# Kernel tuning notes

Hardware: AMD Instinct MI355X
Metric: run time of the kernel (lower is better)

The kernel has to match this reference:

```python
import jax, jax.numpy as jnp
import numpy as np

B, T, D_IN, H, E = 256, 512, 256, 256, 96  # batch, enc seq, input_size, hidden_size, num_embeddings


def setup_inputs() -> dict:
    key = jax.random.key(0)
    ks = jax.random.split(key, 12)
    s = 0.05
    return {
        "prev_h": jax.random.normal(ks[0], (B, H), jnp.float32),
        "prev_c": jax.random.normal(ks[1], (B, H), jnp.float32),
        "batch_H": jax.random.normal(ks[2], (B, T, D_IN), jnp.float32),
        "char_onehots": jax.random.uniform(ks[3], (B, E), jnp.float32),
        "W_i2h": jax.random.normal(ks[4], (H, D_IN), jnp.float32) * s,
        "W_h2h": jax.random.normal(ks[5], (H, H), jnp.float32) * s,
        "b_h2h": jax.random.normal(ks[6], (H,), jnp.float32) * s,
        "W_score": jax.random.normal(ks[7], (1, H), jnp.float32) * s,
        "W_ih": jax.random.normal(ks[8], (4 * H, D_IN + E), jnp.float32) * s,
        "W_hh": jax.random.normal(ks[9], (4 * H, H), jnp.float32) * s,
        "b_ih": jax.random.normal(ks[10], (4 * H,), jnp.float32) * s,
        "b_hh": jax.random.normal(ks[11], (4 * H,), jnp.float32) * s,
    }


def reference(prev_h, prev_c, batch_H, char_onehots,
              W_i2h, W_h2h, b_h2h, W_score, W_ih, W_hh, b_ih, b_hh):
    # additive attention over encoder features
    proj = jnp.einsum('btd,hd->bth', batch_H, W_i2h)          # [B,T,H]
    hid = prev_h @ W_h2h.T + b_h2h                             # [B,H]
    e = jnp.einsum('bth,oh->bto', jnp.tanh(proj + hid[:, None, :]), W_score)  # [B,T,1]
    alpha = jax.nn.softmax(e, axis=1)                          # [B,T,1]
    context = jnp.einsum('bt,btd->bd', alpha[..., 0], batch_H) # [B,D_IN]
    x = jnp.concatenate([context, char_onehots], axis=1)       # [B,D_IN+E]
    # LSTM cell step (PyTorch gate order: i, f, g, o)
    gates = x @ W_ih.T + b_ih + prev_h @ W_hh.T + b_hh         # [B,4H]
    i, f, g, o = jnp.split(gates, 4, axis=1)
    c_new = jax.nn.sigmoid(f) * prev_c + jax.nn.sigmoid(i) * jnp.tanh(g)
    h_new = jax.nn.sigmoid(o) * jnp.tanh(c_new)
    return (h_new, c_new, jnp.swapaxes(alpha, 1, 2))           # alpha -> [B,1,T]
```

## Files before the change

kernel.cpp:

```cpp
#include <hip/hip_runtime.h>

typedef __attribute__((ext_vector_type(8))) short short8;
typedef __attribute__((ext_vector_type(4))) float f32x4;

#define KPAD 40
#define APITCH 264

#define WS_HID   0u
#define WS_P     262144u
#define WS_Z     786432u
#define WS_CTX   794624u
#define WS_CTXP  1056768u
#define WS_WBF   3153920u

__device__ __forceinline__ unsigned cvtpk(float lo, float hi) {
    unsigned r;
    asm("v_cvt_pk_bf16_f32 %0, %1, %2" : "=v"(r) : "v"(lo), "v"(hi));
    return r;
}
__device__ __forceinline__ int4 pack8(float4 x0, float4 x1) {
    int4 q;
    q.x = (int)cvtpk(x0.x, x0.y);
    q.y = (int)cvtpk(x0.z, x0.w);
    q.z = (int)cvtpk(x1.x, x1.y);
    q.w = (int)cvtpk(x1.z, x1.w);
    return q;
}
__device__ __forceinline__ float bf2f(unsigned s) {
    union { float f; unsigned u; } v; v.u = s << 16;
    return v.f;
}
__device__ __forceinline__ float tanh_fast(float x) {
    float e2 = __expf(2.f * x);
    return 1.f - 2.f * __builtin_amdgcn_rcpf(e2 + 1.f);
}
__device__ __forceinline__ float sigmoid_fast(float x) {
    return __builtin_amdgcn_rcpf(1.f + __expf(-x));
}

__global__ __launch_bounds__(256) void k_prep(
    const float* __restrict__ prev_h, const float* __restrict__ W_i2h,
    const float* __restrict__ W_h2h, const float* __restrict__ b_h2h,
    float* __restrict__ hid, short* __restrict__ Wbf)
{
    int bid = blockIdx.x, tid = threadIdx.x;
    if (bid < 256) {
        __shared__ float ph[256];
        ph[tid] = prev_h[bid * 256 + tid];
        __syncthreads();
        float acc = b_h2h[tid];
        const float4* w = (const float4*)(W_h2h + tid * 256);
        #pragma unroll 8
        for (int k4 = 0; k4 < 64; ++k4) {
            float4 ww = w[k4];
            acc += ww.x * ph[k4*4+0] + ww.y * ph[k4*4+1] + ww.z * ph[k4*4+2] + ww.w * ph[k4*4+3];
        }
        hid[bid * 256 + tid] = acc;
    } else {
        int idx = ((bid - 256) * 256 + tid) * 8;
        float4 x0 = *(const float4*)(W_i2h + idx);
        float4 x1 = *(const float4*)(W_i2h + idx + 4);
        *(int4*)&Wbf[idx] = pack8(x0, x1);
    }
}

__global__ __launch_bounds__(256, 2) void k_escore_ctx(
    const float* __restrict__ BH, const short* __restrict__ Wbf,
    const float* __restrict__ hid, const float* __restrict__ Wsc,
    float* __restrict__ p_out, float* __restrict__ zbuf, float* __restrict__ ctxp)
{
    __shared__ short Al[64 * APITCH];
    __shared__ float eps[4 * 64];
    __shared__ float pl[64];
    __shared__ float r4[4 * 256];

    const int tid = threadIdx.x;
    const int lane = tid & 63;
    const int w = tid >> 6;
    const int l15 = lane & 15, lg = lane >> 4;
    const int bt0 = blockIdx.x * 64;
    const int b = bt0 >> 9;
    const int c = blockIdx.x & 7;

    short8 breg[4][8];
    {
        const short* bb = Wbf + (size_t)(w * 64 + l15) * 256 + lg * 8;
        #pragma unroll
        for (int cf = 0; cf < 4; cf++)
            #pragma unroll
            for (int ks = 0; ks < 8; ks++)
                breg[cf][ks] = *(const short8*)(bb + (size_t)cf * 16 * 256 + ks * 32);
    }

    {
        const float* as = BH + (size_t)bt0 * 256 + tid * 8;
        const int row0 = tid >> 5, colw = (tid & 31) * 8;
        #pragma unroll
        for (int i = 0; i < 8; ++i) {
            float4 x0 = *(const float4*)(as + i * 2048);
            float4 x1 = *(const float4*)(as + i * 2048 + 4);
            *(int4*)&Al[(i * 8 + row0) * APITCH + colw] = pack8(x0, x1);
        }
    }
    __syncthreads();

    f32x4 acc[4][4];
    #pragma unroll
    for (int i = 0; i < 4; i++)
        #pragma unroll
        for (int j = 0; j < 4; j++) acc[i][j] = (f32x4){0.f, 0.f, 0.f, 0.f};

    #pragma unroll
    for (int ks = 0; ks < 8; ++ks) {
        short8 af[4];
        #pragma unroll
        for (int rf = 0; rf < 4; rf++)
            af[rf] = *(const short8*)&Al[(rf * 16 + l15) * APITCH + ks * 32 + lg * 8];
        #pragma unroll
        for (int rf = 0; rf < 4; rf++)
            #pragma unroll
            for (int cf = 0; cf < 4; cf++)
                acc[rf][cf] = __builtin_amdgcn_mfma_f32_16x16x32_bf16(af[rf], breg[cf][ks], acc[rf][cf], 0, 0, 0);
    }

    float esum[4][4];
    #pragma unroll
    for (int rf = 0; rf < 4; rf++)
        #pragma unroll
        for (int r = 0; r < 4; r++) esum[rf][r] = 0.f;

    #pragma unroll
    for (int cf = 0; cf < 4; cf++) {
        int col = w * 64 + cf * 16 + l15;
        float wsv = Wsc[col];
        float hd = hid[b * 256 + col];
        #pragma unroll
        for (int rf = 0; rf < 4; rf++)
            #pragma unroll
            for (int r = 0; r < 4; r++)
                esum[rf][r] += wsv * tanh_fast(acc[rf][cf][r] + hd);
    }
    #pragma unroll
    for (int rf = 0; rf < 4; rf++)
        #pragma unroll
        for (int r = 0; r < 4; r++) {
            float s = esum[rf][r];
            s += __shfl_xor(s, 1); s += __shfl_xor(s, 2);
            s += __shfl_xor(s, 4); s += __shfl_xor(s, 8);
            esum[rf][r] = s;
        }
    if (l15 == 0) {
        #pragma unroll
        for (int rf = 0; rf < 4; rf++)
            #pragma unroll
            for (int r = 0; r < 4; r++)
                eps[w * 64 + rf * 16 + lg * 4 + r] = esum[rf][r];
    }
    __syncthreads();

    if (tid < 64) {
        float e = eps[tid] + eps[64 + tid] + eps[128 + tid] + eps[192 + tid];
        float p = __expf(e);
        p_out[bt0 + tid] = p;
        pl[tid] = p;
        float z = p;
        z += __shfl_xor(z, 1); z += __shfl_xor(z, 2); z += __shfl_xor(z, 4);
        z += __shfl_xor(z, 8); z += __shfl_xor(z, 16); z += __shfl_xor(z, 32);
        if (tid == 0) zbuf[blockIdx.x] = z;
    }
    __syncthreads();

    {
        float c0 = 0.f, c1 = 0.f, c2 = 0.f, c3 = 0.f;
        #pragma unroll
        for (int t = 0; t < 16; ++t) {
            int row = w * 16 + t;
            float pv = pl[row];
            unsigned v1 = *(const unsigned*)&Al[row * APITCH + lane * 2];
            unsigned v2 = *(const unsigned*)&Al[row * APITCH + 128 + lane * 2];
            c0 += pv * bf2f(v1 & 0xffffu); c1 += pv * bf2f(v1 >> 16);
            c2 += pv * bf2f(v2 & 0xffffu); c3 += pv * bf2f(v2 >> 16);
        }
        r4[w * 256 + lane * 2]       = c0;
        r4[w * 256 + lane * 2 + 1]   = c1;
        r4[w * 256 + 128 + lane * 2] = c2;
        r4[w * 256 + 129 + lane * 2] = c3;
    }
    __syncthreads();
    ctxp[((size_t)(c * 256 + b)) * 256 + tid] = r4[tid] + r4[256 + tid] + r4[512 + tid] + r4[768 + tid];
}

__global__ __launch_bounds__(256) void k_finalize(
    const float* __restrict__ p, const float* __restrict__ zbuf,
    const float* __restrict__ ctxp, float* __restrict__ alpha, float* __restrict__ ctx)
{
    int b = blockIdx.x, t = threadIdx.x;
    float Z = 0.f;
    #pragma unroll
    for (int cc = 0; cc < 8; ++cc) Z += zbuf[b * 8 + cc];
    float inv = 1.f / Z;
    alpha[b * 512 + t] = p[b * 512 + t] * inv;
    alpha[b * 512 + 256 + t] = p[b * 512 + 256 + t] * inv;
    float s = 0.f;
    #pragma unroll
    for (int cc = 0; cc < 8; ++cc) s += ctxp[((size_t)(cc * 256 + b)) * 256 + t];
    ctx[b * 256 + t] = s * inv;
}

__global__ __launch_bounds__(256) void k_gates_lstm(
    const float* __restrict__ ctx, const float* __restrict__ onehot,
    const float* __restrict__ prev_h, const float* __restrict__ W_ih,
    const float* __restrict__ W_hh, const float* __restrict__ b_ih,
    const float* __restrict__ b_hh, const float* __restrict__ prev_c,
    float* __restrict__ out)
{
    __shared__ char smem[20800];
    short* AlB = (short*)smem;
    short* BlB = (short*)smem + 5120;
    const int tid = threadIdx.x;
    const int lane = tid & 63;
    const int w = tid >> 6;
    const int l15 = lane & 15, lg = lane >> 4;
    const int rb = blockIdx.x * 64;
    const int hb = blockIdx.y;

    f32x4 acc[4];
    #pragma unroll
    for (int j = 0; j < 4; j++) acc[j] = (f32x4){0.f, 0.f, 0.f, 0.f};

    const int arow = tid >> 2, akg = tid & 3;
    const int rg = rb + arow;
    const int bn = tid >> 2, bq = tid & 3;
    const int np_ = hb * 64 + bn, hh_ = np_ >> 2, gg_ = np_ & 3;
    const float* wih_row = W_ih + (size_t)(gg_ * 256 + hh_) * 352;
    const float* whh_row = W_hh + (size_t)(gg_ * 256 + hh_) * 256;

    auto stageAB = [&](int kc, int bu) {
        int k0 = kc * 32 + akg * 8;
        const float4* pa;
        if (k0 < 256)      pa = (const float4*)(ctx    + rg * 256 + k0);
        else if (k0 < 352) pa = (const float4*)(onehot + rg * 96  + (k0 - 256));
        else               pa = (const float4*)(prev_h + rg * 256 + (k0 - 352));
        float4 x0 = pa[0], x1 = pa[1];
        *(int4*)&AlB[bu * 2560 + arow * KPAD + akg * 8] = pack8(x0, x1);
        int kb = kc * 32 + bq * 8;
        const float* pb = (kb < 352) ? (wih_row + kb) : (whh_row + (kb - 352));
        float4 y0 = *(const float4*)pb, y1 = *(const float4*)(pb + 4);
        *(int4*)&BlB[bu * 2560 + bn * KPAD + bq * 8] = pack8(y0, y1);
    };

    stageAB(0, 0);
    __syncthreads();

    for (int kc = 0; kc < 19; ++kc) {
        int cur = kc & 1;
        short8 af = *(const short8*)&AlB[cur * 2560 + (w * 16 + l15) * KPAD + lg * 8];
        short8 bfr[4];
        #pragma unroll
        for (int cf = 0; cf < 4; cf++)
            bfr[cf] = *(const short8*)&BlB[cur * 2560 + (cf * 16 + l15) * KPAD + lg * 8];
        if (kc < 18) stageAB(kc + 1, cur ^ 1);
        #pragma unroll
        for (int cf = 0; cf < 4; cf++)
            acc[cf] = __builtin_amdgcn_mfma_f32_16x16x32_bf16(af, bfr[cf], acc[cf], 0, 0, 0);
        __syncthreads();
    }

    float* Gt = (float*)smem;
    #pragma unroll
    for (int cf = 0; cf < 4; cf++) {
        int col = cf * 16 + l15;
        int np = hb * 64 + col;
        int hg = np >> 2, g = np & 3;
        float bias = b_ih[g * 256 + hg] + b_hh[g * 256 + hg];
        #pragma unroll
        for (int r = 0; r < 4; r++)
            Gt[(w * 16 + lg * 4 + r) * 65 + col] = acc[cf][r] + bias;
    }
    __syncthreads();

    #pragma unroll
    for (int it = 0; it < 4; ++it) {
        int elem = it * 256 + tid;
        int row = elem >> 4, hl = elem & 15;
        float gi = Gt[row * 65 + hl * 4 + 0];
        float gf = Gt[row * 65 + hl * 4 + 1];
        float gg = Gt[row * 65 + hl * 4 + 2];
        float go = Gt[row * 65 + hl * 4 + 3];
        int bg = rb + row, hglob = hb * 16 + hl;
        float cv = sigmoid_fast(gf) * prev_c[bg * 256 + hglob] + sigmoid_fast(gi) * tanh_fast(gg);
        out[bg * 256 + hglob] = sigmoid_fast(go) * tanh_fast(cv);
        out[65536 + bg * 256 + hglob] = cv;
    }
}

extern "C" void kernel_launch(void* const* d_in, const int* in_sizes, int n_in,
                              void* d_out, int out_size, void* d_ws, size_t ws_size,
                              hipStream_t stream) {
    (void)in_sizes; (void)n_in; (void)out_size; (void)ws_size;
    const float* prev_h  = (const float*)d_in[0];
    const float* prev_c  = (const float*)d_in[1];
    const float* batch_H = (const float*)d_in[2];
    const float* onehot  = (const float*)d_in[3];
    const float* W_i2h   = (const float*)d_in[4];
    const float* W_h2h   = (const float*)d_in[5];
    const float* b_h2h   = (const float*)d_in[6];
    const float* W_score = (const float*)d_in[7];
    const float* W_ih    = (const float*)d_in[8];
    const float* W_hh    = (const float*)d_in[9];
    const float* b_ih    = (const float*)d_in[10];
    const float* b_hh    = (const float*)d_in[11];

    char* ws = (char*)d_ws;
    float* hid   = (float*)(ws + WS_HID);
    float* p     = (float*)(ws + WS_P);
    float* zbuf  = (float*)(ws + WS_Z);
    float* ctx   = (float*)(ws + WS_CTX);
    float* ctxp  = (float*)(ws + WS_CTXP);
    short* Wbf   = (short*)(ws + WS_WBF);

    float* out = (float*)d_out;
    float* alpha = out + 131072;

    hipLaunchKernelGGL(k_prep,       dim3(288),    dim3(256), 0, stream,
                       prev_h, W_i2h, W_h2h, b_h2h, hid, Wbf);
    hipLaunchKernelGGL(k_escore_ctx, dim3(2048),   dim3(256), 0, stream,
                       batch_H, Wbf, hid, W_score, p, zbuf, ctxp);
    hipLaunchKernelGGL(k_finalize,   dim3(256),    dim3(256), 0, stream,
                       p, zbuf, ctxp, alpha, ctx);
    hipLaunchKernelGGL(k_gates_lstm, dim3(4, 16),  dim3(256), 0, stream,
                       ctx, onehot, prev_h, W_ih, W_hh, b_ih, b_hh, prev_c, out);
}
```

Baseline: 78.59 us.

## Stage encoder tile as fp32 in LDS via direct global-to-LDS loads with XOR swizzle

The encoder-feature tile is now copied straight from global memory into LDS as fp32 using global_load_lds, with an XOR swizzle on 32-byte chunks, instead of passing through registers and being packed to bf16 before the LDS store. The bf16 conversion moves into the MFMA fragment loads, and the context reduction reads exact fp32 values. This is meant to cut register traffic and overlap the global fetch with the weight register loads. In exchange, LDS use doubles to 64 KB, which may reduce occupancy, and every MFMA step now repeats the conversion work.

```diff
diff --git a/kernel.cpp b/kernel.cpp
--- a/kernel.cpp
+++ b/kernel.cpp
@@ -4,7 +4,6 @@
 typedef __attribute__((ext_vector_type(4))) float f32x4;
 
 #define KPAD 40
-#define APITCH 264
 
 #define WS_HID   0u
 #define WS_P     262144u
@@ -26,16 +25,16 @@
     q.w = (int)cvtpk(x1.z, x1.w);
     return q;
 }
-__device__ __forceinline__ float bf2f(unsigned s) {
-    union { float f; unsigned u; } v; v.u = s << 16;
-    return v.f;
-}
 __device__ __forceinline__ float tanh_fast(float x) {
     float e2 = __expf(2.f * x);
     return 1.f - 2.f * __builtin_amdgcn_rcpf(e2 + 1.f);
 }
 __device__ __forceinline__ float sigmoid_fast(float x) {
     return __builtin_amdgcn_rcpf(1.f + __expf(-x));
+}
+__device__ __forceinline__ void gload16(const void* g, void* l) {
+    __builtin_amdgcn_global_load_lds((const __attribute__((address_space(1))) void*)g,
+                                     (__attribute__((address_space(3))) void*)l, 16, 0, 0);
 }
 
 __global__ __launch_bounds__(256) void k_prep(
@@ -69,7 +68,7 @@
     const float* __restrict__ hid, const float* __restrict__ Wsc,
     float* __restrict__ p_out, float* __restrict__ zbuf, float* __restrict__ ctxp)
 {
-    __shared__ short Al[64 * APITCH];
+    __shared__ float Af[64 * 256];
     __shared__ float eps[4 * 64];
     __shared__ float pl[64];
     __shared__ float r4[4 * 256];
@@ -82,26 +81,35 @@
     const int b = bt0 >> 9;
     const int c = blockIdx.x & 7;
 
-    short8 breg[4][8];
+    {
+        const int ulin = lane >> 1;
+        const int half16 = (lane & 1) * 16;
+        #pragma unroll
+        for (int j = 0; j < 16; ++j) {
+            const int r = j * 4 + w;
+            const char* src = (const char*)(BH + (size_t)(bt0 + r) * 256)
+                            + ((ulin ^ (r & 7)) * 32 + half16);
+            char* dst = (char*)Af + j * 4096 + tid * 16;
+            gload16(src, dst);
+        }
+    }
+
+    int breg[4][8][4];
     {
         const short* bb = Wbf + (size_t)(w * 64 + l15) * 256 + lg * 8;
         #pragma unroll
         for (int cf = 0; cf < 4; cf++)
             #pragma unroll
             for (int ks = 0; ks < 8; ks++)
-                breg[cf][ks] = *(const short8*)(bb + (size_t)cf * 16 * 256 + ks * 32);
-    }
-
-    {
-        const float* as = BH + (size_t)bt0 * 256 + tid * 8;
-        const int row0 = tid >> 5, colw = (tid & 31) * 8;
-        #pragma unroll
-        for (int i = 0; i < 8; ++i) {
-            float4 x0 = *(const float4*)(as + i * 2048);
-            float4 x1 = *(const float4*)(as + i * 2048 + 4);
-            *(int4*)&Al[(i * 8 + row0) * APITCH + colw] = pack8(x0, x1);
-        }
-    }
+                *(int4*)breg[cf][ks] = *(const int4*)(bb + (size_t)cf * 16 * 256 + ks * 32);
+    }
+    #pragma unroll
+    for (int cf = 0; cf < 4; cf++)
+        #pragma unroll
+        for (int ks = 0; ks < 8; ks++)
+            #pragma unroll
+            for (int q = 0; q < 4; q++)
+                asm volatile("" : "+v"(breg[cf][ks][q]));
     __syncthreads();
 
     f32x4 acc[4][4];
@@ -114,13 +122,19 @@
     for (int ks = 0; ks < 8; ++ks) {
         short8 af[4];
         #pragma unroll
+        for (int rf = 0; rf < 4; rf++) {
+            const int r = rf * 16 + l15;
+            const float* ap = &Af[r * 256 + (((ks * 4 + lg) ^ (r & 7)) << 3)];
+            float4 x0 = *(const float4*)ap;
+            float4 x1 = *(const float4*)(ap + 4);
+            *(int4*)&af[rf] = pack8(x0, x1);
+        }
+        #pragma unroll
         for (int rf = 0; rf < 4; rf++)
-            af[rf] = *(const short8*)&Al[(rf * 16 + l15) * APITCH + ks * 32 + lg * 8];
-        #pragma unroll
-        for (int rf = 0; rf < 4; rf++)
             #pragma unroll
             for (int cf = 0; cf < 4; cf++)
-                acc[rf][cf] = __builtin_amdgcn_mfma_f32_16x16x32_bf16(af[rf], breg[cf][ks], acc[rf][cf], 0, 0, 0);
+                acc[rf][cf] = __builtin_amdgcn_mfma_f32_16x16x32_bf16(
+                    af[rf], *(const short8*)breg[cf][ks], acc[rf][cf], 0, 0, 0);
     }
 
     float esum[4][4];
@@ -171,20 +185,20 @@
     __syncthreads();
 
     {
-        float c0 = 0.f, c1 = 0.f, c2 = 0.f, c3 = 0.f;
+        float c4[4] = {0.f, 0.f, 0.f, 0.f};
         #pragma unroll
         for (int t = 0; t < 16; ++t) {
-            int row = w * 16 + t;
-            float pv = pl[row];
-            unsigned v1 = *(const unsigned*)&Al[row * APITCH + lane * 2];
-            unsigned v2 = *(const unsigned*)&Al[row * APITCH + 128 + lane * 2];
-            c0 += pv * bf2f(v1 & 0xffffu); c1 += pv * bf2f(v1 >> 16);
-            c2 += pv * bf2f(v2 & 0xffffu); c3 += pv * bf2f(v2 >> 16);
-        }
-        r4[w * 256 + lane * 2]       = c0;
-        r4[w * 256 + lane * 2 + 1]   = c1;
-        r4[w * 256 + 128 + lane * 2] = c2;
-        r4[w * 256 + 129 + lane * 2] = c3;
+            const int r = w * 16 + t;
+            const float pv = pl[r];
+            #pragma unroll
+            for (int q = 0; q < 4; ++q) {
+                const int f = q * 64 + lane;
+                c4[q] += pv * Af[r * 256 + (((f >> 3) ^ (r & 7)) << 3) + (f & 7)];
+            }
+        }
+        #pragma unroll
+        for (int q = 0; q < 4; ++q)
+            r4[w * 256 + q * 64 + lane] = c4[q];
     }
     __syncthreads();
     ctxp[((size_t)(c * 256 + b)) * 256 + tid] = r4[tid] + r4[256 + tid] + r4[512 + tid] + r4[768 + tid];
```

Result: slower. 85.76 us (+9.1%).

## Restructure attention into persistent per-batch score kernel and separate context pass

Applied to the files above, without the earlier changes.

Replaces the 2048-block score+context kernel with a 256-block kernel where each block handles one batch row and loops over 16 tiles of 32 timesteps. Global loads of the next tile are double-buffered into pre-swizzled MFMA fragment layout in LDS, and the W_i2h weights are pre-permuted so each lane reads its B fragment with one contiguous load. Context is now computed in a separate kernel that re-reads batch_H in fp32, which removes the ctxp partials. The trade-off is a second full read of batch_H and only 256 blocks, which may underfill the GPU.

```diff
diff --git a/kernel.cpp b/kernel.cpp
--- a/kernel.cpp
+++ b/kernel.cpp
@@ -4,14 +4,12 @@
 typedef __attribute__((ext_vector_type(4))) float f32x4;
 
 #define KPAD 40
-#define APITCH 264
-
-#define WS_HID   0u
-#define WS_P     262144u
-#define WS_Z     786432u
-#define WS_CTX   794624u
-#define WS_CTXP  1056768u
-#define WS_WBF   3153920u
+
+#define WS_HID 0u
+#define WS_P   262144u
+#define WS_Z   786432u
+#define WS_CTX 802816u
+#define WS_WBF 1064960u
 
 __device__ __forceinline__ unsigned cvtpk(float lo, float hi) {
     unsigned r;
@@ -26,10 +24,6 @@
     q.w = (int)cvtpk(x1.z, x1.w);
     return q;
 }
-__device__ __forceinline__ float bf2f(unsigned s) {
-    union { float f; unsigned u; } v; v.u = s << 16;
-    return v.f;
-}
 __device__ __forceinline__ float tanh_fast(float x) {
     float e2 = __expf(2.f * x);
     return 1.f - 2.f * __builtin_amdgcn_rcpf(e2 + 1.f);
@@ -41,7 +35,7 @@
 __global__ __launch_bounds__(256) void k_prep(
     const float* __restrict__ prev_h, const float* __restrict__ W_i2h,
     const float* __restrict__ W_h2h, const float* __restrict__ b_h2h,
-    float* __restrict__ hid, short* __restrict__ Wbf)
+    float* __restrict__ hid, int4* __restrict__ Wbf)
 {
     int bid = blockIdx.x, tid = threadIdx.x;
     if (bid < 256) {
@@ -57,154 +51,169 @@
         }
         hid[bid * 256 + tid] = acc;
     } else {
-        int idx = ((bid - 256) * 256 + tid) * 8;
-        float4 x0 = *(const float4*)(W_i2h + idx);
-        float4 x1 = *(const float4*)(W_i2h + idx + 4);
-        *(int4*)&Wbf[idx] = pack8(x0, x1);
-    }
-}
-
-__global__ __launch_bounds__(256, 2) void k_escore_ctx(
-    const float* __restrict__ BH, const short* __restrict__ Wbf,
+        int u = (bid - 256) * 256 + tid;
+        int w = (u >> 11) & 3, cf = (u >> 9) & 3, ks = (u >> 6) & 7;
+        int n = w * 64 + cf * 16 + (u & 15);
+        int k0 = ks * 32 + ((u >> 4) & 3) * 8;
+        float4 x0 = *(const float4*)(W_i2h + n * 256 + k0);
+        float4 x1 = *(const float4*)(W_i2h + n * 256 + k0 + 4);
+        Wbf[u] = pack8(x0, x1);
+    }
+}
+
+__global__ __launch_bounds__(256, 2) void k_e(
+    const float* __restrict__ BH, const int4* __restrict__ Wbf,
     const float* __restrict__ hid, const float* __restrict__ Wsc,
-    float* __restrict__ p_out, float* __restrict__ zbuf, float* __restrict__ ctxp)
+    float* __restrict__ p_out, float* __restrict__ zbuf)
 {
-    __shared__ short Al[64 * APITCH];
-    __shared__ float eps[4 * 64];
-    __shared__ float pl[64];
-    __shared__ float r4[4 * 256];
+    __shared__ short Afrag[2][8192];
+    __shared__ float eps[2][128];
 
     const int tid = threadIdx.x;
     const int lane = tid & 63;
     const int w = tid >> 6;
     const int l15 = lane & 15, lg = lane >> 4;
-    const int bt0 = blockIdx.x * 64;
-    const int b = bt0 >> 9;
-    const int c = blockIdx.x & 7;
+    const int b = blockIdx.x;
 
     short8 breg[4][8];
-    {
-        const short* bb = Wbf + (size_t)(w * 64 + l15) * 256 + lg * 8;
-        #pragma unroll
-        for (int cf = 0; cf < 4; cf++)
-            #pragma unroll
-            for (int ks = 0; ks < 8; ks++)
-                breg[cf][ks] = *(const short8*)(bb + (size_t)cf * 16 * 256 + ks * 32);
-    }
-
-    {
-        const float* as = BH + (size_t)bt0 * 256 + tid * 8;
-        const int row0 = tid >> 5, colw = (tid & 31) * 8;
-        #pragma unroll
-        for (int i = 0; i < 8; ++i) {
-            float4 x0 = *(const float4*)(as + i * 2048);
-            float4 x1 = *(const float4*)(as + i * 2048 + 4);
-            *(int4*)&Al[(i * 8 + row0) * APITCH + colw] = pack8(x0, x1);
-        }
-    }
+    #pragma unroll
+    for (int cf = 0; cf < 4; cf++)
+        #pragma unroll
+        for (int ks = 0; ks < 8; ks++) {
+            const int4* ap = Wbf + (((w * 4 + cf) * 8 + ks) * 64 + lane);
+            asm volatile("global_load_dwordx4 %0, %1, off"
+                         : "=v"(breg[cf][ks]) : "v"(ap));
+        }
+
+    float4 la0[4], la1[4];
+    auto issueA = [&](int t) {
+        const float* base = BH + ((size_t)b * 512 + t * 32) * 256;
+        #pragma unroll
+        for (int q = 0; q < 4; q++) {
+            int u = q * 256 + tid;
+            int row = ((u >> 9) << 4) | (u & 15);
+            int kb = ((u >> 6) & 7) * 32 + ((u >> 4) & 3) * 8;
+            const float* p4 = base + row * 256 + kb;
+            la0[q] = *(const float4*)p4;
+            la1[q] = *(const float4*)(p4 + 4);
+        }
+    };
+    auto writeA = [&](int buf) {
+        #pragma unroll
+        for (int q = 0; q < 4; q++) {
+            int u = q * 256 + tid;
+            *(int4*)&Afrag[buf][u * 8] = pack8(la0[q], la1[q]);
+        }
+    };
+
+    issueA(0);
+    asm volatile("s_waitcnt vmcnt(0)" ::: "memory");
+    #pragma unroll
+    for (int cf = 0; cf < 4; cf++)
+        asm volatile("" : "+v"(breg[cf][0]), "+v"(breg[cf][1]), "+v"(breg[cf][2]),
+                          "+v"(breg[cf][3]), "+v"(breg[cf][4]), "+v"(breg[cf][5]),
+                          "+v"(breg[cf][6]), "+v"(breg[cf][7]));
+    writeA(0);
     __syncthreads();
 
-    f32x4 acc[4][4];
-    #pragma unroll
-    for (int i = 0; i < 4; i++)
-        #pragma unroll
-        for (int j = 0; j < 4; j++) acc[i][j] = (f32x4){0.f, 0.f, 0.f, 0.f};
-
-    #pragma unroll
-    for (int ks = 0; ks < 8; ++ks) {
-        short8 af[4];
-        #pragma unroll
-        for (int rf = 0; rf < 4; rf++)
-            af[rf] = *(const short8*)&Al[(rf * 16 + l15) * APITCH + ks * 32 + lg * 8];
-        #pragma unroll
-        for (int rf = 0; rf < 4; rf++)
-            #pragma unroll
-            for (int cf = 0; cf < 4; cf++)
-                acc[rf][cf] = __builtin_amdgcn_mfma_f32_16x16x32_bf16(af[rf], breg[cf][ks], acc[rf][cf], 0, 0, 0);
-    }
-
-    float esum[4][4];
-    #pragma unroll
-    for (int rf = 0; rf < 4; rf++)
-        #pragma unroll
-        for (int r = 0; r < 4; r++) esum[rf][r] = 0.f;
-
+    float wsv[4], hd4[4];
     #pragma unroll
     for (int cf = 0; cf < 4; cf++) {
         int col = w * 64 + cf * 16 + l15;
-        float wsv = Wsc[col];
-        float hd = hid[b * 256 + col];
-        #pragma unroll
-        for (int rf = 0; rf < 4; rf++)
-            #pragma unroll
-            for (int r = 0; r < 4; r++)
-                esum[rf][r] += wsv * tanh_fast(acc[rf][cf][r] + hd);
-    }
-    #pragma unroll
-    for (int rf = 0; rf < 4; rf++)
-        #pragma unroll
-        for (int r = 0; r < 4; r++) {
-            float s = esum[rf][r];
-            s += __shfl_xor(s, 1); s += __shfl_xor(s, 2);
-            s += __shfl_xor(s, 4); s += __shfl_xor(s, 8);
-            esum[rf][r] = s;
-        }
-    if (l15 == 0) {
-        #pragma unroll
-        for (int rf = 0; rf < 4; rf++)
-            #pragma unroll
-            for (int r = 0; r < 4; r++)
-                eps[w * 64 + rf * 16 + lg * 4 + r] = esum[rf][r];
-    }
+        wsv[cf] = Wsc[col];
+        hd4[cf] = hid[b * 256 + col];
+    }
+
+    for (int t = 0; t < 16; ++t) {
+        const int cur = t & 1;
+        if (t < 15) issueA(t + 1);
+
+        f32x4 acc[2][4];
+        #pragma unroll
+        for (int rf = 0; rf < 2; rf++)
+            #pragma unroll
+            for (int cf = 0; cf < 4; cf++) acc[rf][cf] = (f32x4){0.f, 0.f, 0.f, 0.f};
+
+        #pragma unroll
+        for (int ks = 0; ks < 8; ++ks) {
+            short8 af[2];
+            #pragma unroll
+            for (int rf = 0; rf < 2; rf++)
+                af[rf] = *(const short8*)&Afrag[cur][(((rf * 8 + ks) * 64) + lane) * 8];
+            #pragma unroll
+            for (int rf = 0; rf < 2; rf++)
+                #pragma unroll
+                for (int cf = 0; cf < 4; cf++)
+                    acc[rf][cf] = __builtin_amdgcn_mfma_f32_16x16x32_bf16(
+                        af[rf], breg[cf][ks], acc[rf][cf], 0, 0, 0);
+        }
+
+        float esum[2][4];
+        #pragma unroll
+        for (int rf = 0; rf < 2; rf++)
+            #pragma unroll
+            for (int r = 0; r < 4; r++) esum[rf][r] = 0.f;
+        #pragma unroll
+        for (int cf = 0; cf < 4; cf++)
+            #pragma unroll
+            for (int rf = 0; rf < 2; rf++)
+                #pragma unroll
+                for (int r = 0; r < 4; r++)
+                    esum[rf][r] += wsv[cf] * tanh_fast(acc[rf][cf][r] + hd4[cf]);
+        #pragma unroll
+        for (int rf = 0; rf < 2; rf++)
+            #pragma unroll
+            for (int r = 0; r < 4; r++) {
+                float s = esum[rf][r];
+                s += __shfl_xor(s, 1); s += __shfl_xor(s, 2);
+                s += __shfl_xor(s, 4); s += __shfl_xor(s, 8);
+                esum[rf][r] = s;
+            }
+        if (l15 == 0) {
+            #pragma unroll
+            for (int rf = 0; rf < 2; rf++)
+                #pragma unroll
+                for (int r = 0; r < 4; r++)
+                    eps[cur][w * 32 + rf * 16 + lg * 4 + r] = esum[rf][r];
+        }
+
+        if (t < 15) writeA(cur ^ 1);
+        __syncthreads();
+
+        if (tid < 32) {
+            float e = eps[cur][tid] + eps[cur][32 + tid] + eps[cur][64 + tid] + eps[cur][96 + tid];
+            float p = __expf(e);
+            p_out[b * 512 + t * 32 + tid] = p;
+            float z = p;
+            z += __shfl_xor(z, 1); z += __shfl_xor(z, 2); z += __shfl_xor(z, 4);
+            z += __shfl_xor(z, 8); z += __shfl_xor(z, 16);
+            if (tid == 0) zbuf[b * 16 + t] = z;
+        }
+    }
+}
+
+__global__ __launch_bounds__(256) void k_ctx(
+    const float* __restrict__ p, const float* __restrict__ zbuf,
+    const float* __restrict__ BH, float* __restrict__ alpha, float* __restrict__ ctx)
+{
+    __shared__ float pl[512];
+    __shared__ float zsh[16];
+    int b = blockIdx.x, t = threadIdx.x;
+    if (t < 16) zsh[t] = zbuf[b * 16 + t];
+    pl[t] = p[b * 512 + t];
+    pl[256 + t] = p[b * 512 + 256 + t];
     __syncthreads();
-
-    if (tid < 64) {
-        float e = eps[tid] + eps[64 + tid] + eps[128 + tid] + eps[192 + tid];
-        float p = __expf(e);
-        p_out[bt0 + tid] = p;
-        pl[tid] = p;
-        float z = p;
-        z += __shfl_xor(z, 1); z += __shfl_xor(z, 2); z += __shfl_xor(z, 4);
-        z += __shfl_xor(z, 8); z += __shfl_xor(z, 16); z += __shfl_xor(z, 32);
-        if (tid == 0) zbuf[blockIdx.x] = z;
-    }
-    __syncthreads();
-
-    {
-        float c0 = 0.f, c1 = 0.f, c2 = 0.f, c3 = 0.f;
-        #pragma unroll
-        for (int t = 0; t < 16; ++t) {
-            int row = w * 16 + t;
-            float pv = pl[row];
-            unsigned v1 = *(const unsigned*)&Al[row * APITCH + lane * 2];
-            unsigned v2 = *(const unsigned*)&Al[row * APITCH + 128 + lane * 2];
-            c0 += pv * bf2f(v1 & 0xffffu); c1 += pv * bf2f(v1 >> 16);
-            c2 += pv * bf2f(v2 & 0xffffu); c3 += pv * bf2f(v2 >> 16);
-        }
-        r4[w * 256 + lane * 2]       = c0;
-        r4[w * 256 + lane * 2 + 1]   = c1;
-        r4[w * 256 + 128 + lane * 2] = c2;
-        r4[w * 256 + 129 + lane * 2] = c3;
-    }
-    __syncthreads();
-    ctxp[((size_t)(c * 256 + b)) * 256 + tid] = r4[tid] + r4[256 + tid] + r4[512 + tid] + r4[768 + tid];
-}
-
-__global__ __launch_bounds__(256) void k_finalize(
-    const float* __restrict__ p, const float* __restrict__ zbuf,
-    const float* __restrict__ ctxp, float* __restrict__ alpha, float* __restrict__ ctx)
-{
-    int b = blockIdx.x, t = threadIdx.x;
     float Z = 0.f;
     #pragma unroll
-    for (int cc = 0; cc < 8; ++cc) Z += zbuf[b * 8 + cc];
+    for (int i = 0; i < 16; ++i) Z += zsh[i];
     float inv = 1.f / Z;
-    alpha[b * 512 + t] = p[b * 512 + t] * inv;
-    alpha[b * 512 + 256 + t] = p[b * 512 + 256 + t] * inv;
-    float s = 0.f;
-    #pragma unroll
-    for (int cc = 0; cc < 8; ++cc) s += ctxp[((size_t)(cc * 256 + b)) * 256 + t];
-    ctx[b * 256 + t] = s * inv;
+    alpha[b * 512 + t] = pl[t] * inv;
+    alpha[b * 512 + 256 + t] = pl[256 + t] * inv;
+    const float* bh = BH + (size_t)b * 512 * 256 + t;
+    float acc = 0.f;
+    #pragma unroll 16
+    for (int tt = 0; tt < 512; ++tt) acc += pl[tt] * bh[(size_t)tt * 256];
+    ctx[b * 256 + t] = acc * inv;
 }
 
 __global__ __launch_bounds__(256) void k_gates_lstm(
@@ -316,18 +325,17 @@
     float* p     = (float*)(ws + WS_P);
     float* zbuf  = (float*)(ws + WS_Z);
     float* ctx   = (float*)(ws + WS_CTX);
-    float* ctxp  = (float*)(ws + WS_CTXP);
-    short* Wbf   = (short*)(ws + WS_WBF);
+    int4*  Wbf   = (int4*)(ws + WS_WBF);
 
     float* out = (float*)d_out;
     float* alpha = out + 131072;
 
     hipLaunchKernelGGL(k_prep,       dim3(288),    dim3(256), 0, stream,
                        prev_h, W_i2h, W_h2h, b_h2h, hid, Wbf);
-    hipLaunchKernelGGL(k_escore_ctx, dim3(2048),   dim3(256), 0, stream,
-                       batch_H, Wbf, hid, W_score, p, zbuf, ctxp);
-    hipLaunchKernelGGL(k_finalize,   dim3(256),    dim3(256), 0, stream,
-                       p, zbuf, ctxp, alpha, ctx);
+    hipLaunchKernelGGL(k_e,          dim3(256),    dim3(256), 0, stream,
+                       batch_H, Wbf, hid, W_score, p, zbuf);
+    hipLaunchKernelGGL(k_ctx,        dim3(256),    dim3(256), 0, stream,
+                       p, zbuf, batch_H, alpha, ctx);
     hipLaunchKernelGGL(k_gates_lstm, dim3(4, 16),  dim3(256), 0, stream,
                        ctx, onehot, prev_h, W_ih, W_hh, b_ih, b_hh, prev_c, out);
 }
```

New measurement: 80.19 us. 1.02x slower.
